# Kernel tuning notes

Hardware: AMD Instinct MI355X
Metric: run time of the kernel (lower is better)

## Reference

```python
import jax, jax.numpy as jnp
import numpy as np

D_MODEL = 1024
D_HIDDEN = 4096
NUM_EXPERTS = 8
B, T = 2, 2048


def setup_inputs() -> dict:
    key = jax.random.key(0)
    ks = jax.random.split(key, 8)
    s = 0.02
    x = jax.random.normal(ks[0], (B, T, D_MODEL), dtype=jnp.float32)
    Wg = jax.random.normal(ks[1], (D_MODEL, NUM_EXPERTS), dtype=jnp.float32) * s
    bg = jnp.zeros((NUM_EXPERTS,), dtype=jnp.float32)
    W1 = jax.random.normal(ks[2], (NUM_EXPERTS, D_MODEL, D_HIDDEN), dtype=jnp.float32) * s
    b1 = jnp.zeros((NUM_EXPERTS, D_HIDDEN), dtype=jnp.float32)
    W2 = jax.random.normal(ks[3], (NUM_EXPERTS, D_HIDDEN, D_MODEL), dtype=jnp.float32) * s
    b2 = jnp.zeros((NUM_EXPERTS, D_MODEL), dtype=jnp.float32)
    return {"x": x, "Wg": Wg, "bg": bg, "W1": W1, "b1": b1, "W2": W2, "b2": b2}


def reference(x, Wg, bg, W1, b1, W2, b2):
    # Gating: top-1 routing
    gate_logits = jnp.einsum('btd,de->bte', x, Wg) + bg          # (B,T,E)
    gate_scores = jax.nn.softmax(gate_logits, axis=-1)
    top1_idx = jnp.argmax(gate_scores, axis=-1)                   # (B,T)
    top1_mask = jax.nn.one_hot(top1_idx, NUM_EXPERTS, dtype=x.dtype)  # (B,T,E)
    top1_weight = jnp.sum(gate_scores * top1_mask, axis=-1, keepdims=True)  # (B,T,1)

    # Dense all-expert compute (faithful to the naive original), then mask.
    # For unselected tokens the original computes expert(0)*0 = 0, identical
    # to expert(x)*0 = 0 here.
    h = jax.nn.silu(jnp.einsum('btd,edh->bteh', x, W1) + b1)      # (B,T,E,H)
    o = jnp.einsum('bteh,ehd->bted', h, W2) + b2                  # (B,T,E,D)
    y = jnp.sum(o * top1_mask[..., None], axis=2) * top1_weight   # (B,T,D)
    return y
```

## Files before the change

kernel.cpp:

```cpp
#include <hip/hip_runtime.h>
#include <stdint.h>

#define D_MODEL 1024
#define D_HIDDEN 4096
#define NUM_EXPERTS 8
#define NTOK 4096
#define MAXSLOT 40
#define KSPLIT 4

typedef __bf16 bf16x8 __attribute__((ext_vector_type(8)));
typedef float floatx4 __attribute__((ext_vector_type(4)));

static __device__ __forceinline__ unsigned short f2bf(float f) {
    union { float f; unsigned int i; } v;
    v.f = f;
    unsigned int i = v.i;
    unsigned int r = (i + 0x7fffu + ((i >> 16) & 1u)) >> 16;
    return (unsigned short)r;
}

__global__ __launch_bounds__(256) void gate_kernel(
    const float* __restrict__ x,
    const float* __restrict__ Wg,
    const float* __restrict__ bg,
    int* __restrict__ counts,
    int* __restrict__ tlist,
    float* __restrict__ wgt)
{
    const int wave = threadIdx.x >> 6;
    const int lane = threadIdx.x & 63;
    const int tok = blockIdx.x * 4 + wave;

    float acc[NUM_EXPERTS];
#pragma unroll
    for (int e = 0; e < NUM_EXPERTS; e++) acc[e] = 0.f;

    const float* xr = x + (size_t)tok * D_MODEL;
    for (int d = lane; d < D_MODEL; d += 64) {
        float xv = xr[d];
        const float4* wr = (const float4*)(Wg + (size_t)d * NUM_EXPERTS);
        float4 w0 = wr[0], w1 = wr[1];
        acc[0] += xv * w0.x; acc[1] += xv * w0.y;
        acc[2] += xv * w0.z; acc[3] += xv * w0.w;
        acc[4] += xv * w1.x; acc[5] += xv * w1.y;
        acc[6] += xv * w1.z; acc[7] += xv * w1.w;
    }
#pragma unroll
    for (int e = 0; e < NUM_EXPERTS; e++) {
        float v = acc[e];
#pragma unroll
        for (int off = 32; off > 0; off >>= 1) v += __shfl_xor(v, off, 64);
        acc[e] = v;
    }
    if (lane == 0) {
        float lg[NUM_EXPERTS];
#pragma unroll
        for (int e = 0; e < NUM_EXPERTS; e++) lg[e] = acc[e] + bg[e];
        int amax = 0;
        float m = lg[0];
#pragma unroll
        for (int e = 1; e < NUM_EXPERTS; e++) {
            if (lg[e] > m) { m = lg[e]; amax = e; }
        }
        float s = 0.f;
#pragma unroll
        for (int e = 0; e < NUM_EXPERTS; e++) s += __expf(lg[e] - m);
        wgt[tok] = 1.0f / s;
        int pos = atomicAdd(&counts[amax], 1);
        tlist[amax * NTOK + pos] = tok;
    }
}

__device__ __forceinline__ bool slot_to_expert(const int* counts, int slot,
                                               int& e_out, int& mt_out, int& cnt_out) {
    int cum = 0;
    for (int i = 0; i < NUM_EXPERTS; i++) {
        int c = counts[i];
        int t = (c + 127) >> 7;
        if (slot < cum + t) {
            e_out = i; mt_out = slot - cum; cnt_out = c;
            return true;
        }
        cum += t;
    }
    return false;
}

__global__ __launch_bounds__(256) void ffn1_kernel(
    const float* __restrict__ x,
    const float* __restrict__ W1,
    const float* __restrict__ b1,
    const int* __restrict__ counts,
    const int* __restrict__ tlist,
    unsigned short* __restrict__ h)
{
    int e, mt, cnt;
    if (!slot_to_expert(counts, blockIdx.y, e, mt, cnt)) return;
    const int n0 = blockIdx.x * 128;

    __shared__ __align__(16) unsigned short As[128][40];
    __shared__ __align__(16) unsigned short Bs[128][40];
    __shared__ int toks[128];

    const int tid = threadIdx.x;
    if (tid < 128) {
        int r = mt * 128 + tid;
        toks[tid] = (r < cnt) ? tlist[e * NTOK + r] : -1;
    }
    __syncthreads();

    const int wave = tid >> 6, lane = tid & 63;
    const int quad = lane >> 4, lm = lane & 15;
    const int mo = (wave & 1) * 64, no = (wave >> 1) * 64;

    floatx4 acc[4][4];
#pragma unroll
    for (int i = 0; i < 4; i++)
#pragma unroll
        for (int j = 0; j < 4; j++) acc[i][j] = (floatx4){0.f, 0.f, 0.f, 0.f};

    const float* W1e = W1 + (size_t)e * D_MODEL * D_HIDDEN;

    const int arow = tid >> 1, ahalf = tid & 1;
    int atok = toks[arow];
    const float* aptr = x + (size_t)(atok < 0 ? 0 : atok) * D_MODEL + ahalf * 16;
    const int bn = tid & 127, bg0 = tid >> 7;

    for (int k0 = 0; k0 < D_MODEL; k0 += 32) {
        float4 a4[4];
#pragma unroll
        for (int i = 0; i < 4; i++) a4[i] = ((const float4*)(aptr + k0))[i];
        unsigned short av[16];
#pragma unroll
        for (int i = 0; i < 4; i++) {
            av[i * 4 + 0] = f2bf(a4[i].x); av[i * 4 + 1] = f2bf(a4[i].y);
            av[i * 4 + 2] = f2bf(a4[i].z); av[i * 4 + 3] = f2bf(a4[i].w);
        }
        *(uint4*)(&As[arow][ahalf * 16])     = ((const uint4*)av)[0];
        *(uint4*)(&As[arow][ahalf * 16 + 8]) = ((const uint4*)av)[1];

#pragma unroll
        for (int t = 0; t < 2; t++) {
            int g = bg0 + t * 2;
            const float* bp = W1e + (size_t)(k0 + g * 8) * D_HIDDEN + n0 + bn;
            unsigned short bv[8];
#pragma unroll
            for (int j = 0; j < 8; j++) bv[j] = f2bf(bp[(size_t)j * D_HIDDEN]);
            *(uint4*)(&Bs[bn][g * 8]) = *(const uint4*)bv;
        }
        __syncthreads();

        bf16x8 af[4], bfr[4];
#pragma unroll
        for (int i = 0; i < 4; i++) {
            af[i]  = *(const bf16x8*)(&As[mo + i * 16 + lm][quad * 8]);
            bfr[i] = *(const bf16x8*)(&Bs[no + i * 16 + lm][quad * 8]);
        }
#pragma unroll
        for (int mi = 0; mi < 4; mi++)
#pragma unroll
            for (int ni = 0; ni < 4; ni++)
                acc[mi][ni] = __builtin_amdgcn_mfma_f32_16x16x32_bf16(
                    af[mi], bfr[ni], acc[mi][ni], 0, 0, 0);
        __syncthreads();
    }

    const float* b1e = b1 + (size_t)e * D_HIDDEN;
#pragma unroll
    for (int ni = 0; ni < 4; ni++) {
        int n = n0 + no + ni * 16 + lm;
        float bias = b1e[n];
#pragma unroll
        for (int mi = 0; mi < 4; mi++)
#pragma unroll
            for (int r = 0; r < 4; r++) {
                int m = mo + mi * 16 + quad * 4 + r;
                int tk = toks[m];
                if (tk >= 0) {
                    float z = acc[mi][ni][r] + bias;
                    h[(size_t)tk * D_HIDDEN + n] = f2bf(z / (1.f + __expf(-z)));
                }
            }
    }
}

__global__ __launch_bounds__(256) void ffn2_kernel(
    const unsigned short* __restrict__ h,
    const float* __restrict__ W2,
    const float* __restrict__ b2,
    const int* __restrict__ counts,
    const int* __restrict__ tlist,
    const float* __restrict__ wgt,
    float* __restrict__ out)
{
    int e, mt, cnt;
    if (!slot_to_expert(counts, blockIdx.y, e, mt, cnt)) return;
    const int n0 = blockIdx.x * 128;
    const int kc = blockIdx.z;
    const int kbeg = kc * (D_HIDDEN / KSPLIT);
    const int kend = kbeg + (D_HIDDEN / KSPLIT);

    __shared__ __align__(16) unsigned short As[128][40];
    __shared__ __align__(16) unsigned short Bs[128][40];
    __shared__ int toks[128];

    const int tid = threadIdx.x;
    if (tid < 128) {
        int r = mt * 128 + tid;
        toks[tid] = (r < cnt) ? tlist[e * NTOK + r] : -1;
    }
    __syncthreads();

    const int wave = tid >> 6, lane = tid & 63;
    const int quad = lane >> 4, lm = lane & 15;
    const int mo = (wave & 1) * 64, no = (wave >> 1) * 64;

    floatx4 acc[4][4];
#pragma unroll
    for (int i = 0; i < 4; i++)
#pragma unroll
        for (int j = 0; j < 4; j++) acc[i][j] = (floatx4){0.f, 0.f, 0.f, 0.f};

    const float* W2e = W2 + (size_t)e * D_HIDDEN * D_MODEL;

    const int arow = tid >> 1, ahalf = tid & 1;
    int atok = toks[arow];
    const unsigned short* aptr =
        h + (size_t)(atok < 0 ? 0 : atok) * D_HIDDEN + ahalf * 16;
    const int bn = tid & 127, bg0 = tid >> 7;

    for (int k0 = kbeg; k0 < kend; k0 += 32) {
        uint4 a0 = *(const uint4*)(aptr + k0);
        uint4 a1 = *(const uint4*)(aptr + k0 + 8);
        *(uint4*)(&As[arow][ahalf * 16])     = a0;
        *(uint4*)(&As[arow][ahalf * 16 + 8]) = a1;

#pragma unroll
        for (int t = 0; t < 2; t++) {
            int g = bg0 + t * 2;
            const float* bp = W2e + (size_t)(k0 + g * 8) * D_MODEL + n0 + bn;
            unsigned short bv[8];
#pragma unroll
            for (int j = 0; j < 8; j++) bv[j] = f2bf(bp[(size_t)j * D_MODEL]);
            *(uint4*)(&Bs[bn][g * 8]) = *(const uint4*)bv;
        }
        __syncthreads();

        bf16x8 af[4], bfr[4];
#pragma unroll
        for (int i = 0; i < 4; i++) {
            af[i]  = *(const bf16x8*)(&As[mo + i * 16 + lm][quad * 8]);
            bfr[i] = *(const bf16x8*)(&Bs[no + i * 16 + lm][quad * 8]);
        }
#pragma unroll
        for (int mi = 0; mi < 4; mi++)
#pragma unroll
            for (int ni = 0; ni < 4; ni++)
                acc[mi][ni] = __builtin_amdgcn_mfma_f32_16x16x32_bf16(
                    af[mi], bfr[ni], acc[mi][ni], 0, 0, 0);
        __syncthreads();
    }

    const float* b2e = b2 + (size_t)e * D_MODEL;
#pragma unroll
    for (int ni = 0; ni < 4; ni++) {
        int n = n0 + no + ni * 16 + lm;
        float bias = (kc == 0) ? b2e[n] : 0.f;
#pragma unroll
        for (int mi = 0; mi < 4; mi++)
#pragma unroll
            for (int r = 0; r < 4; r++) {
                int m = mo + mi * 16 + quad * 4 + r;
                int tk = toks[m];
                if (tk >= 0) {
                    atomicAdd(&out[(size_t)tk * D_MODEL + n],
                              (acc[mi][ni][r] + bias) * wgt[tk]);
                }
            }
    }
}

extern "C" void kernel_launch(void* const* d_in, const int* in_sizes, int n_in,
                              void* d_out, int out_size, void* d_ws, size_t ws_size,
                              hipStream_t stream) {
    const float* x  = (const float*)d_in[0];
    const float* Wg = (const float*)d_in[1];
    const float* bg = (const float*)d_in[2];
    const float* W1 = (const float*)d_in[3];
    const float* b1 = (const float*)d_in[4];
    const float* W2 = (const float*)d_in[5];
    const float* b2 = (const float*)d_in[6];
    float* out = (float*)d_out;

    char* ws = (char*)d_ws;
    int*   counts = (int*)ws;
    float* wgt    = (float*)(ws + 1024);
    int*   tlist  = (int*)(ws + 32768);
    unsigned short* h = (unsigned short*)(ws + 262144);

    hipMemsetAsync(counts, 0, NUM_EXPERTS * sizeof(int), stream);
    hipMemsetAsync(out, 0, (size_t)out_size * sizeof(float), stream);

    gate_kernel<<<NTOK / 4, 256, 0, stream>>>(x, Wg, bg, counts, tlist, wgt);
    ffn1_kernel<<<dim3(D_HIDDEN / 128, MAXSLOT), 256, 0, stream>>>(x, W1, b1, counts, tlist, h);
    ffn2_kernel<<<dim3(D_MODEL / 128, MAXSLOT, KSPLIT), 256, 0, stream>>>(h, W2, b2, counts, tlist, wgt, out);
}
```

Measured before the change: 574.7 us.

## Pre-transpose weights to bf16 and stage tiles with async global-to-LDS loads

Adds a per-call kernel that converts W1 and W2 to bf16 and transposes them to N-major in workspace. The FFN kernels then load weight tiles, and in ffn2 the hidden activations too, using 16-byte global_load_lds copies straight into unpadded LDS, in place of strided fp32 loads converted per element. The aim is to cut strided global traffic and VALU conversion work in the GEMM inner loops. The cost is an extra full pass over about 268MB of fp32 weights plus bf16 writes on every call, and the unpadded LDS layout may cause bank conflicts. The old path remains as a fallback when the workspace is too small.

```diff
diff --git a/kernel.cpp b/kernel.cpp
--- a/kernel.cpp
+++ b/kernel.cpp
@@ -11,6 +11,13 @@
 typedef __bf16 bf16x8 __attribute__((ext_vector_type(8)));
 typedef float floatx4 __attribute__((ext_vector_type(4)));
 
+typedef const __attribute__((address_space(1))) void* gas_t;
+typedef __attribute__((address_space(3))) void* las_t;
+
+static __device__ __forceinline__ void async_copy16(const void* g, void* l) {
+    __builtin_amdgcn_global_load_lds((gas_t)g, (las_t)l, 16, 0, 0);
+}
+
 static __device__ __forceinline__ unsigned short f2bf(float f) {
     union { float f; unsigned int i; } v;
     v.f = f;
@@ -20,12 +27,9 @@
 }
 
 __global__ __launch_bounds__(256) void gate_kernel(
-    const float* __restrict__ x,
-    const float* __restrict__ Wg,
-    const float* __restrict__ bg,
-    int* __restrict__ counts,
-    int* __restrict__ tlist,
-    float* __restrict__ wgt)
+    const float* __restrict__ x, const float* __restrict__ Wg,
+    const float* __restrict__ bg, int* __restrict__ counts,
+    int* __restrict__ tlist, float* __restrict__ wgt)
 {
     const int wave = threadIdx.x >> 6;
     const int lane = threadIdx.x & 63;
@@ -71,6 +75,35 @@
     }
 }
 
+__global__ __launch_bounds__(256) void cvt_transpose(
+    const float* __restrict__ W, unsigned short* __restrict__ Wt,
+    int K, int N)
+{
+    __shared__ unsigned short tile[64][68];
+    const float* We = W + (size_t)blockIdx.z * K * N;
+    unsigned short* Wte = Wt + (size_t)blockIdx.z * K * N;
+    const int kb = blockIdx.y * 64, nb = blockIdx.x * 64;
+    const int t = threadIdx.x;
+
+    const int kr = t >> 4, nc = (t & 15) * 4;
+#pragma unroll
+    for (int s = 0; s < 4; s++) {
+        int k = kr + s * 16;
+        float4 v = *(const float4*)(We + (size_t)(kb + k) * N + nb + nc);
+        unsigned short p[4] = {f2bf(v.x), f2bf(v.y), f2bf(v.z), f2bf(v.w)};
+        *(uint2*)(&tile[k][nc]) = *(const uint2*)p;
+    }
+    __syncthreads();
+
+    const int n = t >> 2, kc = (t & 3) * 16;
+    unsigned short o[16];
+#pragma unroll
+    for (int j = 0; j < 16; j++) o[j] = tile[kc + j][n];
+    unsigned short* dst = Wte + (size_t)(nb + n) * K + kb + kc;
+    *(uint4*)(dst)     = ((const uint4*)o)[0];
+    *(uint4*)(dst + 8) = ((const uint4*)o)[1];
+}
+
 __device__ __forceinline__ bool slot_to_expert(const int* counts, int slot,
                                                int& e_out, int& mt_out, int& cnt_out) {
     int cum = 0;
@@ -86,9 +119,10 @@
     return false;
 }
 
-__global__ __launch_bounds__(256) void ffn1_kernel(
+
+__global__ __launch_bounds__(256) void ffn1_fast(
     const float* __restrict__ x,
-    const float* __restrict__ W1,
+    const unsigned short* __restrict__ W1t,
     const float* __restrict__ b1,
     const int* __restrict__ counts,
     const int* __restrict__ tlist,
@@ -98,8 +132,8 @@
     if (!slot_to_expert(counts, blockIdx.y, e, mt, cnt)) return;
     const int n0 = blockIdx.x * 128;
 
-    __shared__ __align__(16) unsigned short As[128][40];
-    __shared__ __align__(16) unsigned short Bs[128][40];
+    __shared__ __align__(16) unsigned short As[128 * 32];
+    __shared__ __align__(16) unsigned short Bs[128 * 32];
     __shared__ int toks[128];
 
     const int tid = threadIdx.x;
@@ -119,14 +153,23 @@
 #pragma unroll
         for (int j = 0; j < 4; j++) acc[i][j] = (floatx4){0.f, 0.f, 0.f, 0.f};
 
-    const float* W1e = W1 + (size_t)e * D_MODEL * D_HIDDEN;
+    const unsigned short* W1te = W1t + (size_t)e * D_MODEL * D_HIDDEN;
 
     const int arow = tid >> 1, ahalf = tid & 1;
     int atok = toks[arow];
     const float* aptr = x + (size_t)(atok < 0 ? 0 : atok) * D_MODEL + ahalf * 16;
-    const int bn = tid & 127, bg0 = tid >> 7;
+    const int brb0 = wave * 32;
+    const int brl = lane >> 2;
+    const int bkp = (lane & 3) * 8;
 
     for (int k0 = 0; k0 < D_MODEL; k0 += 32) {
+#pragma unroll
+        for (int i = 0; i < 2; i++) {
+            int rb = brb0 + i * 16;
+            const unsigned short* gp =
+                W1te + (size_t)(n0 + rb + brl) * D_MODEL + k0 + bkp;
+            async_copy16(gp, &Bs[rb * 32]);
+        }
         float4 a4[4];
 #pragma unroll
         for (int i = 0; i < 4; i++) a4[i] = ((const float4*)(aptr + k0))[i];
@@ -136,25 +179,15 @@
             av[i * 4 + 0] = f2bf(a4[i].x); av[i * 4 + 1] = f2bf(a4[i].y);
             av[i * 4 + 2] = f2bf(a4[i].z); av[i * 4 + 3] = f2bf(a4[i].w);
         }
-        *(uint4*)(&As[arow][ahalf * 16])     = ((const uint4*)av)[0];
-        *(uint4*)(&As[arow][ahalf * 16 + 8]) = ((const uint4*)av)[1];
-
-#pragma unroll
-        for (int t = 0; t < 2; t++) {
-            int g = bg0 + t * 2;
-            const float* bp = W1e + (size_t)(k0 + g * 8) * D_HIDDEN + n0 + bn;
-            unsigned short bv[8];
-#pragma unroll
-            for (int j = 0; j < 8; j++) bv[j] = f2bf(bp[(size_t)j * D_HIDDEN]);
-            *(uint4*)(&Bs[bn][g * 8]) = *(const uint4*)bv;
-        }
+        *(uint4*)(&As[arow * 32 + ahalf * 16])     = ((const uint4*)av)[0];
+        *(uint4*)(&As[arow * 32 + ahalf * 16 + 8]) = ((const uint4*)av)[1];
         __syncthreads();
 
         bf16x8 af[4], bfr[4];
 #pragma unroll
         for (int i = 0; i < 4; i++) {
-            af[i]  = *(const bf16x8*)(&As[mo + i * 16 + lm][quad * 8]);
-            bfr[i] = *(const bf16x8*)(&Bs[no + i * 16 + lm][quad * 8]);
+            af[i]  = *(const bf16x8*)(&As[(mo + i * 16 + lm) * 32 + quad * 8]);
+            bfr[i] = *(const bf16x8*)(&Bs[(no + i * 16 + lm) * 32 + quad * 8]);
         }
 #pragma unroll
         for (int mi = 0; mi < 4; mi++)
@@ -184,9 +217,9 @@
     }
 }
 
-__global__ __launch_bounds__(256) void ffn2_kernel(
+__global__ __launch_bounds__(256) void ffn2_fast(
     const unsigned short* __restrict__ h,
-    const float* __restrict__ W2,
+    const unsigned short* __restrict__ W2t,
     const float* __restrict__ b2,
     const int* __restrict__ counts,
     const int* __restrict__ tlist,
@@ -196,12 +229,11 @@
     int e, mt, cnt;
     if (!slot_to_expert(counts, blockIdx.y, e, mt, cnt)) return;
     const int n0 = blockIdx.x * 128;
-    const int kc = blockIdx.z;
-    const int kbeg = kc * (D_HIDDEN / KSPLIT);
+    const int kbeg = blockIdx.z * (D_HIDDEN / KSPLIT);
     const int kend = kbeg + (D_HIDDEN / KSPLIT);
 
-    __shared__ __align__(16) unsigned short As[128][40];
-    __shared__ __align__(16) unsigned short Bs[128][40];
+    __shared__ __align__(16) unsigned short As[128 * 32];
+    __shared__ __align__(16) unsigned short Bs[128 * 32];
     __shared__ int toks[128];
 
     const int tid = threadIdx.x;
@@ -221,20 +253,187 @@
 #pragma unroll
         for (int j = 0; j < 4; j++) acc[i][j] = (floatx4){0.f, 0.f, 0.f, 0.f};
 
+    const unsigned short* W2te = W2t + (size_t)e * D_HIDDEN * D_MODEL;
+
+    const int rb0 = wave * 32;
+    const int rl = lane >> 2;
+    const int kp = (lane & 3) * 8;
+
+    int ta0 = toks[rb0 + rl];        if (ta0 < 0) ta0 = 0;
+    int ta1 = toks[rb0 + 16 + rl];   if (ta1 < 0) ta1 = 0;
+    const unsigned short* ap0 = h + (size_t)ta0 * D_HIDDEN + kp;
+    const unsigned short* ap1 = h + (size_t)ta1 * D_HIDDEN + kp;
+
+    for (int k0 = kbeg; k0 < kend; k0 += 32) {
+        async_copy16(ap0 + k0, &As[rb0 * 32]);
+        async_copy16(ap1 + k0, &As[(rb0 + 16) * 32]);
+#pragma unroll
+        for (int i = 0; i < 2; i++) {
+            int rb = rb0 + i * 16;
+            const unsigned short* gp =
+                W2te + (size_t)(n0 + rb + rl) * D_HIDDEN + k0 + kp;
+            async_copy16(gp, &Bs[rb * 32]);
+        }
+        __syncthreads();
+
+        bf16x8 af[4], bfr[4];
+#pragma unroll
+        for (int i = 0; i < 4; i++) {
+            af[i]  = *(const bf16x8*)(&As[(mo + i * 16 + lm) * 32 + quad * 8]);
+            bfr[i] = *(const bf16x8*)(&Bs[(no + i * 16 + lm) * 32 + quad * 8]);
+        }
+#pragma unroll
+        for (int mi = 0; mi < 4; mi++)
+#pragma unroll
+            for (int ni = 0; ni < 4; ni++)
+                acc[mi][ni] = __builtin_amdgcn_mfma_f32_16x16x32_bf16(
+                    af[mi], bfr[ni], acc[mi][ni], 0, 0, 0);
+        __syncthreads();
+    }
+
+    const float* b2e = b2 + (size_t)e * D_MODEL;
+#pragma unroll
+    for (int ni = 0; ni < 4; ni++) {
+        int n = n0 + no + ni * 16 + lm;
+        float bias = (blockIdx.z == 0) ? b2e[n] : 0.f;
+#pragma unroll
+        for (int mi = 0; mi < 4; mi++)
+#pragma unroll
+            for (int r = 0; r < 4; r++) {
+                int m = mo + mi * 16 + quad * 4 + r;
+                int tk = toks[m];
+                if (tk >= 0) {
+                    atomicAdd(&out[(size_t)tk * D_MODEL + n],
+                              (acc[mi][ni][r] + bias) * wgt[tk]);
+                }
+            }
+    }
+}
+
+__global__ __launch_bounds__(256) void ffn1_fb(
+    const float* __restrict__ x, const float* __restrict__ W1,
+    const float* __restrict__ b1, const int* __restrict__ counts,
+    const int* __restrict__ tlist, unsigned short* __restrict__ h)
+{
+    int e, mt, cnt;
+    if (!slot_to_expert(counts, blockIdx.y, e, mt, cnt)) return;
+    const int n0 = blockIdx.x * 128;
+    __shared__ __align__(16) unsigned short As[128][40];
+    __shared__ __align__(16) unsigned short Bs[128][40];
+    __shared__ int toks[128];
+    const int tid = threadIdx.x;
+    if (tid < 128) {
+        int r = mt * 128 + tid;
+        toks[tid] = (r < cnt) ? tlist[e * NTOK + r] : -1;
+    }
+    __syncthreads();
+    const int wave = tid >> 6, lane = tid & 63;
+    const int quad = lane >> 4, lm = lane & 15;
+    const int mo = (wave & 1) * 64, no = (wave >> 1) * 64;
+    floatx4 acc[4][4];
+#pragma unroll
+    for (int i = 0; i < 4; i++)
+#pragma unroll
+        for (int j = 0; j < 4; j++) acc[i][j] = (floatx4){0.f, 0.f, 0.f, 0.f};
+    const float* W1e = W1 + (size_t)e * D_MODEL * D_HIDDEN;
+    const int arow = tid >> 1, ahalf = tid & 1;
+    int atok = toks[arow];
+    const float* aptr = x + (size_t)(atok < 0 ? 0 : atok) * D_MODEL + ahalf * 16;
+    const int bn = tid & 127, bg0 = tid >> 7;
+    for (int k0 = 0; k0 < D_MODEL; k0 += 32) {
+        float4 a4[4];
+#pragma unroll
+        for (int i = 0; i < 4; i++) a4[i] = ((const float4*)(aptr + k0))[i];
+        unsigned short av[16];
+#pragma unroll
+        for (int i = 0; i < 4; i++) {
+            av[i * 4 + 0] = f2bf(a4[i].x); av[i * 4 + 1] = f2bf(a4[i].y);
+            av[i * 4 + 2] = f2bf(a4[i].z); av[i * 4 + 3] = f2bf(a4[i].w);
+        }
+        *(uint4*)(&As[arow][ahalf * 16])     = ((const uint4*)av)[0];
+        *(uint4*)(&As[arow][ahalf * 16 + 8]) = ((const uint4*)av)[1];
+#pragma unroll
+        for (int t = 0; t < 2; t++) {
+            int g = bg0 + t * 2;
+            const float* bp = W1e + (size_t)(k0 + g * 8) * D_HIDDEN + n0 + bn;
+            unsigned short bv[8];
+#pragma unroll
+            for (int j = 0; j < 8; j++) bv[j] = f2bf(bp[(size_t)j * D_HIDDEN]);
+            *(uint4*)(&Bs[bn][g * 8]) = *(const uint4*)bv;
+        }
+        __syncthreads();
+        bf16x8 af[4], bfr[4];
+#pragma unroll
+        for (int i = 0; i < 4; i++) {
+            af[i]  = *(const bf16x8*)(&As[mo + i * 16 + lm][quad * 8]);
+            bfr[i] = *(const bf16x8*)(&Bs[no + i * 16 + lm][quad * 8]);
+        }
+#pragma unroll
+        for (int mi = 0; mi < 4; mi++)
+#pragma unroll
+            for (int ni = 0; ni < 4; ni++)
+                acc[mi][ni] = __builtin_amdgcn_mfma_f32_16x16x32_bf16(
+                    af[mi], bfr[ni], acc[mi][ni], 0, 0, 0);
+        __syncthreads();
+    }
+    const float* b1e = b1 + (size_t)e * D_HIDDEN;
+#pragma unroll
+    for (int ni = 0; ni < 4; ni++) {
+        int n = n0 + no + ni * 16 + lm;
+        float bias = b1e[n];
+#pragma unroll
+        for (int mi = 0; mi < 4; mi++)
+#pragma unroll
+            for (int r = 0; r < 4; r++) {
+                int m = mo + mi * 16 + quad * 4 + r;
+                int tk = toks[m];
+                if (tk >= 0) {
+                    float z = acc[mi][ni][r] + bias;
+                    h[(size_t)tk * D_HIDDEN + n] = f2bf(z / (1.f + __expf(-z)));
+                }
+            }
+    }
+}
+
+__global__ __launch_bounds__(256) void ffn2_fb(
+    const unsigned short* __restrict__ h, const float* __restrict__ W2,
+    const float* __restrict__ b2, const int* __restrict__ counts,
+    const int* __restrict__ tlist, const float* __restrict__ wgt,
+    float* __restrict__ out)
+{
+    int e, mt, cnt;
+    if (!slot_to_expert(counts, blockIdx.y, e, mt, cnt)) return;
+    const int n0 = blockIdx.x * 128;
+    const int kbeg = blockIdx.z * (D_HIDDEN / KSPLIT);
+    const int kend = kbeg + (D_HIDDEN / KSPLIT);
+    __shared__ __align__(16) unsigned short As[128][40];
+    __shared__ __align__(16) unsigned short Bs[128][40];
+    __shared__ int toks[128];
+    const int tid = threadIdx.x;
+    if (tid < 128) {
+        int r = mt * 128 + tid;
+        toks[tid] = (r < cnt) ? tlist[e * NTOK + r] : -1;
+    }
+    __syncthreads();
+    const int wave = tid >> 6, lane = tid & 63;
+    const int quad = lane >> 4, lm = lane & 15;
+    const int mo = (wave & 1) * 64, no = (wave >> 1) * 64;
+    floatx4 acc[4][4];
+#pragma unroll
+    for (int i = 0; i < 4; i++)
+#pragma unroll
+        for (int j = 0; j < 4; j++) acc[i][j] = (floatx4){0.f, 0.f, 0.f, 0.f};
     const float* W2e = W2 + (size_t)e * D_HIDDEN * D_MODEL;
-
     const int arow = tid >> 1, ahalf = tid & 1;
     int atok = toks[arow];
     const unsigned short* aptr =
         h + (size_t)(atok < 0 ? 0 : atok) * D_HIDDEN + ahalf * 16;
     const int bn = tid & 127, bg0 = tid >> 7;
-
     for (int k0 = kbeg; k0 < kend; k0 += 32) {
         uint4 a0 = *(const uint4*)(aptr + k0);
         uint4 a1 = *(const uint4*)(aptr + k0 + 8);
         *(uint4*)(&As[arow][ahalf * 16])     = a0;
         *(uint4*)(&As[arow][ahalf * 16 + 8]) = a1;
-
 #pragma unroll
         for (int t = 0; t < 2; t++) {
             int g = bg0 + t * 2;
@@ -245,7 +444,6 @@
             *(uint4*)(&Bs[bn][g * 8]) = *(const uint4*)bv;
         }
         __syncthreads();
-
         bf16x8 af[4], bfr[4];
 #pragma unroll
         for (int i = 0; i < 4; i++) {
@@ -260,12 +458,11 @@
                     af[mi], bfr[ni], acc[mi][ni], 0, 0, 0);
         __syncthreads();
     }
-
     const float* b2e = b2 + (size_t)e * D_MODEL;
 #pragma unroll
     for (int ni = 0; ni < 4; ni++) {
         int n = n0 + no + ni * 16 + lm;
-        float bias = (kc == 0) ? b2e[n] : 0.f;
+        float bias = (blockIdx.z == 0) ? b2e[n] : 0.f;
 #pragma unroll
         for (int mi = 0; mi < 4; mi++)
 #pragma unroll
@@ -297,11 +494,28 @@
     float* wgt    = (float*)(ws + 1024);
     int*   tlist  = (int*)(ws + 32768);
     unsigned short* h = (unsigned short*)(ws + 262144);
+    unsigned short* W1t = (unsigned short*)(ws + 33816576);
+    unsigned short* W2t = (unsigned short*)(ws + 100925440);
+    const size_t WS_NEEDED = 168034304;
 
     hipMemsetAsync(counts, 0, NUM_EXPERTS * sizeof(int), stream);
     hipMemsetAsync(out, 0, (size_t)out_size * sizeof(float), stream);
 
     gate_kernel<<<NTOK / 4, 256, 0, stream>>>(x, Wg, bg, counts, tlist, wgt);
-    ffn1_kernel<<<dim3(D_HIDDEN / 128, MAXSLOT), 256, 0, stream>>>(x, W1, b1, counts, tlist, h);
-    ffn2_kernel<<<dim3(D_MODEL / 128, MAXSLOT, KSPLIT), 256, 0, stream>>>(h, W2, b2, counts, tlist, wgt, out);
-}
+
+    if (ws_size >= WS_NEEDED) {
+        cvt_transpose<<<dim3(D_HIDDEN / 64, D_MODEL / 64, NUM_EXPERTS), 256, 0, stream>>>(
+            W1, W1t, D_MODEL, D_HIDDEN);
+        cvt_transpose<<<dim3(D_MODEL / 64, D_HIDDEN / 64, NUM_EXPERTS), 256, 0, stream>>>(
+            W2, W2t, D_HIDDEN, D_MODEL);
+        ffn1_fast<<<dim3(D_HIDDEN / 128, MAXSLOT), 256, 0, stream>>>(
+            x, W1t, b1, counts, tlist, h);
+        ffn2_fast<<<dim3(D_MODEL / 128, MAXSLOT, KSPLIT), 256, 0, stream>>>(
+            h, W2t, b2, counts, tlist, wgt, out);
+    } else {
+        ffn1_fb<<<dim3(D_HIDDEN / 128, MAXSLOT), 256, 0, stream>>>(
+            x, W1, b1, counts, tlist, h);
+        ffn2_fb<<<dim3(D_MODEL / 128, MAXSLOT, KSPLIT), 256, 0, stream>>>(
+            h, W2, b2, counts, tlist, wgt, out);
+    }
+}
```

Measured after the change: 624.6 us. +8.7%, slower.
